# Kernel tuning notes

Measured on AMD Instinct MI355X. Metric: run time of the kernel, lower is better.

The kernel has to match this reference:

```python
import jax, jax.numpy as jnp
import numpy as np

N_NODES = 100000
N_EDGES = 1600000
N_GRAPHS = 256
D = 128
L = 3
N_OUT = 10


def setup_inputs() -> dict:
    key = jax.random.key(0)
    ks = jax.random.split(key, 6)
    x = jax.random.normal(ks[0], (N_NODES, D), dtype=jnp.float32)
    edge_index = jax.random.randint(ks[1], (2, N_EDGES), 0, N_NODES, dtype=jnp.int64)
    batch = jnp.sort(jax.random.randint(ks[2], (N_NODES,), 0, N_GRAPHS, dtype=jnp.int64))
    conv_w = jax.random.normal(ks[3], (L, D, D), dtype=jnp.float32) * (1.0 / np.sqrt(D))
    conv_b = jnp.zeros((L, D), dtype=jnp.float32)
    out_w = jax.random.normal(ks[4], (3 * D, N_OUT), dtype=jnp.float32) * (1.0 / np.sqrt(3 * D))
    out_b = jnp.zeros((N_OUT,), dtype=jnp.float32)
    return {"x": x, "edge_index": edge_index, "batch": batch,
            "conv_w": conv_w, "conv_b": conv_b, "out_w": out_w, "out_b": out_b}


def reference(x, edge_index, batch, conv_w, conv_b, out_w, out_b):
    N = x.shape[0]
    # --- add self-loops (PyG GCNConv default) ---
    loop = jnp.arange(N, dtype=edge_index.dtype)
    src = jnp.concatenate([edge_index[0], loop])  # [E+N]
    dst = jnp.concatenate([edge_index[1], loop])
    # --- symmetric normalization: deg computed on dst (col) ---
    deg = jax.ops.segment_sum(jnp.ones_like(dst, dtype=x.dtype), dst, num_segments=N)
    dinv = jnp.where(deg > 0, jax.lax.rsqrt(jnp.maximum(deg, 1.0)), 0.0)
    norm = dinv[src] * dinv[dst]  # [E+N]

    h = x
    for l in range(conv_w.shape[0]):
        h = h @ conv_w[l]                                   # [N, D] transform first
        msg = h[src] * norm[:, None]                        # gather + scale
        h = jax.ops.segment_sum(msg, dst, num_segments=N)   # scatter-add
        h = jax.nn.relu(h + conv_b[l])

    # --- global max / mean / add pooling over graphs ---
    B = N_GRAPHS
    gmax = jax.ops.segment_max(h, batch, num_segments=B)
    gsum = jax.ops.segment_sum(h, batch, num_segments=B)
    cnt = jax.ops.segment_sum(jnp.ones((N, 1), h.dtype), batch, num_segments=B)
    gmean = gsum / jnp.maximum(cnt, 1.0)
    pooled = jnp.concatenate([gmax, gmean, gsum], axis=1)   # [B, 3D]
    # dropout p=0.5 is identity in eval mode
    return pooled @ out_w + out_b
```

## Files before the change

kernel.cpp:

```cpp
#include <hip/hip_runtime.h>
#include <hip/hip_bf16.h>

#define D 128
#define NP 8
#define DPB 64
#define KPB (DPB * NP)
#define SUB 64
#define CAP_SUB 64

typedef __attribute__((ext_vector_type(8))) __bf16 bf16x8;
typedef __attribute__((ext_vector_type(4))) float f32x4;
typedef __attribute__((ext_vector_type(4))) short s16x4;
typedef __attribute__((ext_vector_type(8))) short s16x8;

static __device__ __forceinline__ short f2bf(float f) {
    union { float f; unsigned u; } in; in.f = f;
    unsigned u = in.u;
    u += 0x7fffu + ((u >> 16) & 1u);
    return (short)(u >> 16);
}

__global__ void k_bucket(const int* __restrict__ src, const int* __restrict__ dst,
                         int* __restrict__ bcnt, int* __restrict__ staging,
                         int E, int KBE) {
    int i = blockIdx.x * 256 + threadIdx.x;
    if (i >= E) return;
    int d = dst[i], s = src[i];
    int b = d >> 6;
    int key = ((d & 63) << 3) | (s >> 14);
    int j = blockIdx.x & (SUB - 1);
    int slot = atomicAdd(&bcnt[j * KBE + b], 1);
    if (slot < CAP_SUB) staging[((size_t)j * KBE + b) * CAP_SUB + slot] = (key << 17) | s;
}

__global__ void k_btot(const int* __restrict__ bcnt, int* __restrict__ btot, int KBE) {
    int b = blockIdx.x * 256 + threadIdx.x;
    if (b >= KBE) return;
    int v = 0;
    #pragma unroll
    for (int j = 0; j < SUB; j++) {
        int c = bcnt[j * KBE + b];
        v += (c > CAP_SUB) ? CAP_SUB : c;
    }
    btot[b] = v;
}

__global__ void k_bscan(const int* __restrict__ btot, int* __restrict__ bbase,
                        int* __restrict__ row_ptr, int nkeys, int KBE) {
    __shared__ int sm[512];
    __shared__ int carry;
    int t = threadIdx.x;
    if (t == 0) carry = 0;
    __syncthreads();
    for (int c0 = 0; c0 < KBE; c0 += 512) {
        int b = c0 + t;
        int v = (b < KBE) ? btot[b] : 0;
        sm[t] = v;
        __syncthreads();
        for (int off = 1; off < 512; off <<= 1) {
            int x = (t >= off) ? sm[t - off] : 0;
            __syncthreads();
            sm[t] += x;
            __syncthreads();
        }
        if (b < KBE) bbase[b] = sm[t] - v + carry;
        __syncthreads();
        if (t == 0) carry += sm[511];
        __syncthreads();
    }
    if (t == 0) { bbase[KBE] = carry; row_ptr[nkeys] = carry; }
}

__global__ __launch_bounds__(256) void k_build(
    const int* __restrict__ staging, const int* __restrict__ bcnt,
    const int* __restrict__ bbase, int* __restrict__ row_ptr,
    int* __restrict__ csr_src, float* __restrict__ dinv, int N, int KBE)
{
    const int b = blockIdx.x;
    const int tid = threadIdx.x;
    __shared__ int cnt[KPB];
    __shared__ int subn[SUB];
    __shared__ int chunkbuf[256];
    __shared__ int carry;

    if (tid < SUB) {
        int c = bcnt[tid * KBE + b];
        subn[tid] = (c > CAP_SUB) ? CAP_SUB : c;
    }
    for (int k = tid; k < KPB; k += 256) cnt[k] = 0;
    if (tid == 0) carry = 0;
    __syncthreads();

    const int base = bbase[b];
    const int nb = bbase[b + 1] - base;
    const int j = tid >> 2, l4 = tid & 3;
    const int* __restrict__ sreg = staging + ((size_t)j * KBE + b) * CAP_SUB;
    const int sn = subn[j];

    for (int e = l4; e < sn; e += 4)
        atomicAdd(&cnt[sreg[e] >> 17], 1);
    __syncthreads();

    #pragma unroll 1
    for (int c = 0; c < KPB / 256; c++) {
        int idx = c * 256 + tid;
        int v = cnt[idx];
        chunkbuf[tid] = v;
        __syncthreads();
        for (int off = 1; off < 256; off <<= 1) {
            int x = (tid >= off) ? chunkbuf[tid - off] : 0;
            __syncthreads();
            chunkbuf[tid] += x;
            __syncthreads();
        }
        cnt[idx] = chunkbuf[tid] - v + carry;
        __syncthreads();
        if (tid == 255) carry += chunkbuf[255];
        __syncthreads();
    }

    for (int k = tid; k < KPB; k += 256)
        row_ptr[(size_t)b * KPB + k] = base + cnt[k];
    for (int dl = tid; dl < DPB; dl += 256) {
        int d = b * DPB + dl;
        if (d < N) {
            int hi2 = (dl == DPB - 1) ? nb : cnt[(dl + 1) * NP];
            int deg = hi2 - cnt[dl * NP];
            dinv[d] = rsqrtf((float)deg + 1.0f);
        }
    }
    __syncthreads();

    for (int e = l4; e < sn; e += 4) {
        int w = sreg[e];
        int slot = base + atomicAdd(&cnt[w >> 17], 1);
        csr_src[slot] = w & 0x1FFFF;
    }
}

__global__ void k_gseg(const int* __restrict__ batch, int* __restrict__ gstart,
                       int* __restrict__ gcnt, int N, int B) {
    int g = blockIdx.x * blockDim.x + threadIdx.x;
    if (g > B) return;
    int lo = 0, hi = N;
    while (lo < hi) {
        int mid = (lo + hi) >> 1;
        if (batch[mid] < g) lo = mid + 1; else hi = mid;
    }
    gstart[g] = lo;
    if (g < B) {
        int lo2 = lo, hi2 = N;
        while (lo2 < hi2) {
            int mid = (lo2 + hi2) >> 1;
            if (batch[mid] < g + 1) lo2 = mid + 1; else hi2 = mid;
        }
        gcnt[g] = lo2 - lo;
    }
}

__global__ void k_cvt_x(const float* __restrict__ x, const float* __restrict__ dinv,
                        short* __restrict__ xb, int total4) {
    int i = blockIdx.x * blockDim.x + threadIdx.x;
    if (i < total4) {
        float d = dinv[i >> 5];
        float4 v = ((const float4*)x)[i];
        s16x4 o;
        o.x = f2bf(v.x * d); o.y = f2bf(v.y * d);
        o.z = f2bf(v.z * d); o.w = f2bf(v.w * d);
        ((s16x4*)xb)[i] = o;
    }
}

__global__ void k_cvt_w(const float* __restrict__ W, short* __restrict__ Wt, int total) {
    int i = blockIdx.x * blockDim.x + threadIdx.x;
    if (i < total) {
        int l = i >> 14;
        int rem = i & 16383;
        int n = rem >> 7;
        int k = rem & 127;
        Wt[i] = f2bf(W[(l << 14) + (k << 7) + n]);
    }
}

__global__ __launch_bounds__(256) void k_layer(
    const short* __restrict__ hin, const int* __restrict__ row_ptr,
    const int* __restrict__ csr_src, const float* __restrict__ dinv,
    const short* __restrict__ Wt, const float* __restrict__ bias,
    short* __restrict__ hout, float* __restrict__ hrelu, int N, int mode)
{
    __shared__ __align__(16) short tile[16 * 128];
    const int tid = threadIdx.x;
    const int wave = tid >> 6;
    const int lane = tid & 63;
    const int group = lane >> 4;
    const int lg = lane & 15;
    const int off = lg * 8;
    const int node_base = blockIdx.x * 16;
    const int r = wave * 4 + group;
    const int i = node_base + r;

    short* dstp = &tile[r * 128 + ((lg ^ (r & 7)) << 3)];
    if (i < N) {
        float acc[8];
        bf16x8 v = *(const bf16x8*)(hin + (size_t)i * D + off);
        #pragma unroll
        for (int k = 0; k < 8; k++) acc[k] = (float)v[k];

        int t = row_ptr[i * NP];
        const int end = row_ptr[i * NP + NP];
        const int nfull = (end - t) >> 3;

        int i0, i1, i2, i3, i4, i5, i6, i7;
        if (nfull > 0) {
            i0 = csr_src[t + 0]; i1 = csr_src[t + 1];
            i2 = csr_src[t + 2]; i3 = csr_src[t + 3];
            i4 = csr_src[t + 4]; i5 = csr_src[t + 5];
            i6 = csr_src[t + 6]; i7 = csr_src[t + 7];
        }
        #pragma unroll 1
        for (int c = 0; c < nfull; c++) {
            bf16x8 v0 = *(const bf16x8*)(hin + (size_t)i0 * D + off);
            bf16x8 v1 = *(const bf16x8*)(hin + (size_t)i1 * D + off);
            bf16x8 v2 = *(const bf16x8*)(hin + (size_t)i2 * D + off);
            bf16x8 v3 = *(const bf16x8*)(hin + (size_t)i3 * D + off);
            bf16x8 v4 = *(const bf16x8*)(hin + (size_t)i4 * D + off);
            bf16x8 v5 = *(const bf16x8*)(hin + (size_t)i5 * D + off);
            bf16x8 v6 = *(const bf16x8*)(hin + (size_t)i6 * D + off);
            bf16x8 v7 = *(const bf16x8*)(hin + (size_t)i7 * D + off);
            t += 8;
            if (c + 1 < nfull) {
                i0 = csr_src[t + 0]; i1 = csr_src[t + 1];
                i2 = csr_src[t + 2]; i3 = csr_src[t + 3];
                i4 = csr_src[t + 4]; i5 = csr_src[t + 5];
                i6 = csr_src[t + 6]; i7 = csr_src[t + 7];
            }
            #pragma unroll
            for (int k = 0; k < 8; k++)
                acc[k] += ((((float)v0[k] + (float)v1[k]) + ((float)v2[k] + (float)v3[k]))
                         + (((float)v4[k] + (float)v5[k]) + ((float)v6[k] + (float)v7[k])));
        }
        for (; t + 4 <= end; t += 4) {
            int j0 = csr_src[t + 0], j1 = csr_src[t + 1];
            int j2 = csr_src[t + 2], j3 = csr_src[t + 3];
            bf16x8 v0 = *(const bf16x8*)(hin + (size_t)j0 * D + off);
            bf16x8 v1 = *(const bf16x8*)(hin + (size_t)j1 * D + off);
            bf16x8 v2 = *(const bf16x8*)(hin + (size_t)j2 * D + off);
            bf16x8 v3 = *(const bf16x8*)(hin + (size_t)j3 * D + off);
            #pragma unroll
            for (int k = 0; k < 8; k++)
                acc[k] += (((float)v0[k] + (float)v1[k]) + ((float)v2[k] + (float)v3[k]));
        }
        for (; t < end; t++) {
            int j0 = csr_src[t];
            bf16x8 v0 = *(const bf16x8*)(hin + (size_t)j0 * D + off);
            #pragma unroll
            for (int k = 0; k < 8; k++) acc[k] += (float)v0[k];
        }

        const float di = dinv[i];
        s16x8 o;
        #pragma unroll
        for (int k = 0; k < 8; k++) o[k] = f2bf(acc[k] * di);
        *(s16x8*)dstp = o;
    } else {
        s16x8 z = {0, 0, 0, 0, 0, 0, 0, 0};
        *(s16x8*)dstp = z;
    }
    __syncthreads();

    bf16x8 afrag[4];
    #pragma unroll
    for (int kt = 0; kt < 4; kt++)
        afrag[kt] = *(const bf16x8*)(&tile[lg * 128 + (((group + 4 * kt) ^ (lg & 7)) << 3)]);

    f32x4 acc2[2];
    #pragma unroll
    for (int nt = 0; nt < 2; nt++) { f32x4 z = {0.f, 0.f, 0.f, 0.f}; acc2[nt] = z; }
    #pragma unroll
    for (int nt = 0; nt < 2; nt++) {
        const short* bp = Wt + (size_t)(wave * 32 + nt * 16 + lg) * D + group * 8;
        #pragma unroll
        for (int kt = 0; kt < 4; kt++) {
            bf16x8 b = *(const bf16x8*)(bp + kt * 32);
            acc2[nt] = __builtin_amdgcn_mfma_f32_16x16x32_bf16(afrag[kt], b, acc2[nt], 0, 0, 0);
        }
    }

    float bcol[2];
    #pragma unroll
    for (int nt = 0; nt < 2; nt++) bcol[nt] = bias[wave * 32 + nt * 16 + lg];
    const int row0 = node_base + group * 4;
    #pragma unroll
    for (int i2 = 0; i2 < 4; i2++) {
        int r2 = row0 + i2;
        if (r2 < N) {
            if (mode == 0) {
                float dr = dinv[r2];
                #pragma unroll
                for (int nt = 0; nt < 2; nt++) {
                    int col = wave * 32 + nt * 16 + lg;
                    float val = fmaxf(acc2[nt][i2] + bcol[nt], 0.0f);
                    hout[(size_t)r2 * D + col] = f2bf(val * dr);
                }
            } else {
                #pragma unroll
                for (int nt = 0; nt < 2; nt++) {
                    int col = wave * 32 + nt * 16 + lg;
                    hrelu[(size_t)r2 * D + col] = fmaxf(acc2[nt][i2] + bcol[nt], 0.0f);
                }
            }
        }
    }
}

__global__ __launch_bounds__(256) void k_pool(const float* __restrict__ hrelu,
                                              const int* __restrict__ gstart,
                                              const int* __restrict__ gcnt,
                                              float* __restrict__ pmax,
                                              float* __restrict__ psum, int B) {
    int g = blockIdx.x >> 2;
    int q = blockIdx.x & 3;
    int c = threadIdx.x & 127;
    int p = threadIdx.x >> 7;
    int start = gstart[g];
    int endr = start + gcnt[g];

    float mx0 = 0.f, mx1 = 0.f, sm0 = 0.f, sm1 = 0.f;
    int r = start + q * 2 + p;
    for (; r + 8 < endr; r += 16) {
        float v0 = hrelu[(size_t)r * D + c];
        float v1 = hrelu[(size_t)(r + 8) * D + c];
        mx0 = fmaxf(mx0, v0); sm0 += v0;
        mx1 = fmaxf(mx1, v1); sm1 += v1;
    }
    if (r < endr) {
        float v0 = hrelu[(size_t)r * D + c];
        mx0 = fmaxf(mx0, v0); sm0 += v0;
    }
    float mx = fmaxf(mx0, mx1), sm = sm0 + sm1;

    __shared__ float smx[128], ssm[128];
    if (p == 1) { smx[c] = mx; ssm[c] = sm; }
    __syncthreads();
    if (p == 0) {
        pmax[((size_t)q * B + g) * D + c] = fmaxf(mx, smx[c]);
        psum[((size_t)q * B + g) * D + c] = sm + ssm[c];
    }
}

__global__ void k_final(const float* __restrict__ pmax, const float* __restrict__ psum,
                        const int* __restrict__ gcnt, const float* __restrict__ ow,
                        const float* __restrict__ ob, float* __restrict__ out, int B) {
    int g = blockIdx.x;
    int t = threadIdx.x;
    float part[10];
    #pragma unroll
    for (int o = 0; o < 10; o++) part[o] = 0.f;
    float invc = 1.0f / fmaxf((float)gcnt[g], 1.0f);
    for (int k = t; k < 3 * D; k += 64) {
        int c = (k < D) ? k : ((k < 2 * D) ? k - D : k - 2 * D);
        float pk;
        if (k < D) {
            float m = pmax[(size_t)g * D + c];
            #pragma unroll
            for (int q = 1; q < 4; q++) m = fmaxf(m, pmax[((size_t)q * B + g) * D + c]);
            pk = m;
        } else {
            float s = psum[(size_t)g * D + c];
            #pragma unroll
            for (int q = 1; q < 4; q++) s += psum[((size_t)q * B + g) * D + c];
            pk = (k < 2 * D) ? s * invc : s;
        }
        const float* w = ow + k * 10;
        #pragma unroll
        for (int o = 0; o < 10; o++) part[o] += pk * w[o];
    }
    #pragma unroll
    for (int off = 32; off > 0; off >>= 1)
        #pragma unroll
        for (int o = 0; o < 10; o++) part[o] += __shfl_down(part[o], off, 64);
    if (t == 0)
        #pragma unroll
        for (int o = 0; o < 10; o++) out[g * 10 + o] = part[o] + ob[o];
}

extern "C" void kernel_launch(void* const* d_in, const int* in_sizes, int n_in,
                              void* d_out, int out_size, void* d_ws, size_t ws_size,
                              hipStream_t stream) {
    const float* x     = (const float*)d_in[0];
    const int*   ei    = (const int*)d_in[1];
    const int*   batch = (const int*)d_in[2];
    const float* convw = (const float*)d_in[3];
    const float* convb = (const float*)d_in[4];
    const float* outw  = (const float*)d_in[5];
    const float* outb  = (const float*)d_in[6];
    float* out = (float*)d_out;

    const int N = in_sizes[0] / D;
    const int E = in_sizes[1] / 2;
    const int L = in_sizes[3] / (D * D);
    const int B = out_size / 10;

    const int* src = ei;
    const int* dst = ei + E;

    const int KBE   = (N + DPB - 1) / DPB;
    const int nkeys = KBE * KPB;

    char* p = (char*)d_ws;
    auto alloc = [&](size_t bytes) { char* r = p; p += (bytes + 255) & ~255ull; return r; };
    short* hb0     = (short*)alloc((size_t)N * D * 2);
    short* hb1     = (short*)alloc((size_t)N * D * 2);
    float* hrelu   = (float*)alloc((size_t)N * D * 4);
    short* Wt      = (short*)alloc((size_t)L * D * D * 2);
    int*   row_ptr = (int*)alloc(((size_t)nkeys + 1) * 4);
    int*   csr_src = (int*)alloc((size_t)E * 4);
    int*   bcnt    = (int*)alloc((size_t)SUB * KBE * 4);
    int*   btot    = (int*)alloc((size_t)KBE * 4);
    int*   bbase   = (int*)alloc(((size_t)KBE + 1) * 4);
    float* dinv    = (float*)alloc((size_t)N * 4);
    float* pmax    = (float*)alloc((size_t)4 * B * D * 4);
    float* psum    = (float*)alloc((size_t)4 * B * D * 4);
    int*   gcnt    = (int*)alloc((size_t)B * 4);
    int*   gstart  = (int*)alloc(((size_t)B + 1) * 4);

    int* staging = (int*)hrelu;

    hipMemsetAsync(bcnt, 0, (size_t)SUB * KBE * 4, stream);

    k_bucket<<<(E + 255) / 256, 256, 0, stream>>>(src, dst, bcnt, staging, E, KBE);
    k_gseg<<<1, 512, 0, stream>>>(batch, gstart, gcnt, N, B);
    k_btot<<<(KBE + 255) / 256, 256, 0, stream>>>(bcnt, btot, KBE);
    k_bscan<<<1, 512, 0, stream>>>(btot, bbase, row_ptr, nkeys, KBE);
    k_build<<<KBE, 256, 0, stream>>>(staging, bcnt, bbase, row_ptr, csr_src, dinv, N, KBE);
    k_cvt_x<<<((N * D / 4) + 255) / 256, 256, 0, stream>>>(x, dinv, hb0, N * D / 4);
    k_cvt_w<<<((L * D * D) + 255) / 256, 256, 0, stream>>>(convw, Wt, L * D * D);

    const int lblocks = (N + 15) / 16;
    k_layer<<<lblocks, 256, 0, stream>>>(hb0, row_ptr, csr_src, dinv, Wt,
                                         convb, hb1, hrelu, N, 0);
    k_layer<<<lblocks, 256, 0, stream>>>(hb1, row_ptr, csr_src, dinv, Wt + D * D,
                                         convb + D, hb0, hrelu, N, 0);
    k_layer<<<lblocks, 256, 0, stream>>>(hb0, row_ptr, csr_src, dinv, Wt + 2 * D * D,
                                         convb + 2 * D, hb1, hrelu, N, 1);

    k_pool<<<B * 4, 256, 0, stream>>>(hrelu, gstart, gcnt, pmax, psum, B);
    k_final<<<B, 64, 0, stream>>>(pmax, psum, gcnt, outw, outb, out, B);
}
```

Before: 458.1 us.

## Replace bucketed source-sorted CSR build with plain histogram-scan-scatter CSR

```diff
diff --git a/kernel.cpp b/kernel.cpp
--- a/kernel.cpp
+++ b/kernel.cpp
@@ -2,11 +2,6 @@
 #include <hip/hip_bf16.h>
 
 #define D 128
-#define NP 8
-#define DPB 64
-#define KPB (DPB * NP)
-#define SUB 64
-#define CAP_SUB 64
 
 typedef __attribute__((ext_vector_type(8))) __bf16 bf16x8;
 typedef __attribute__((ext_vector_type(4))) float f32x4;
@@ -20,122 +15,64 @@
     return (short)(u >> 16);
 }
 
-__global__ void k_bucket(const int* __restrict__ src, const int* __restrict__ dst,
-                         int* __restrict__ bcnt, int* __restrict__ staging,
-                         int E, int KBE) {
+
+__global__ void k_hist(const int* __restrict__ dst, int* __restrict__ cnt, int E) {
+    int i = blockIdx.x * 256 + threadIdx.x;
+    if (i < E) atomicAdd(&cnt[dst[i]], 1);
+}
+
+__global__ void k_scan1(const int* __restrict__ cnt, int* __restrict__ row_ptr,
+                        int* __restrict__ part, int N) {
+    __shared__ int sm[256];
+    const int t = threadIdx.x;
+    const int i = blockIdx.x * 256 + t;
+    int v = (i < N) ? cnt[i] : 0;
+    sm[t] = v;
+    __syncthreads();
+    for (int off = 1; off < 256; off <<= 1) {
+        int x = (t >= off) ? sm[t - off] : 0;
+        __syncthreads();
+        sm[t] += x;
+        __syncthreads();
+    }
+    if (i < N) row_ptr[i] = sm[t] - v;
+    if (t == 255) part[blockIdx.x] = sm[255];
+}
+
+__global__ void k_scan2(int* __restrict__ part, int nb) {
+    __shared__ int sm[512];
+    const int t = threadIdx.x;
+    int v = (t < nb) ? part[t] : 0;
+    sm[t] = v;
+    __syncthreads();
+    for (int off = 1; off < 512; off <<= 1) {
+        int x = (t >= off) ? sm[t - off] : 0;
+        __syncthreads();
+        sm[t] += x;
+        __syncthreads();
+    }
+    if (t < nb) part[t] = sm[t] - v;
+}
+
+__global__ void k_scan3(const int* __restrict__ cnt, int* __restrict__ row_ptr,
+                        const int* __restrict__ part, int* __restrict__ cur,
+                        float* __restrict__ dinv, int N, int E) {
+    const int i = blockIdx.x * 256 + threadIdx.x;
+    if (i < N) {
+        int r = row_ptr[i] + part[blockIdx.x];
+        row_ptr[i] = r;
+        cur[i] = r;
+        dinv[i] = rsqrtf((float)cnt[i] + 1.0f);
+    }
+    if (blockIdx.x == 0 && threadIdx.x == 0) row_ptr[N] = E;
+}
+
+__global__ void k_scatter(const int* __restrict__ src, const int* __restrict__ dst,
+                          int* __restrict__ cur, int* __restrict__ csr_src, int E) {
     int i = blockIdx.x * 256 + threadIdx.x;
     if (i >= E) return;
-    int d = dst[i], s = src[i];
-    int b = d >> 6;
-    int key = ((d & 63) << 3) | (s >> 14);
-    int j = blockIdx.x & (SUB - 1);
-    int slot = atomicAdd(&bcnt[j * KBE + b], 1);
-    if (slot < CAP_SUB) staging[((size_t)j * KBE + b) * CAP_SUB + slot] = (key << 17) | s;
-}
-
-__global__ void k_btot(const int* __restrict__ bcnt, int* __restrict__ btot, int KBE) {
-    int b = blockIdx.x * 256 + threadIdx.x;
-    if (b >= KBE) return;
-    int v = 0;
-    #pragma unroll
-    for (int j = 0; j < SUB; j++) {
-        int c = bcnt[j * KBE + b];
-        v += (c > CAP_SUB) ? CAP_SUB : c;
-    }
-    btot[b] = v;
-}
-
-__global__ void k_bscan(const int* __restrict__ btot, int* __restrict__ bbase,
-                        int* __restrict__ row_ptr, int nkeys, int KBE) {
-    __shared__ int sm[512];
-    __shared__ int carry;
-    int t = threadIdx.x;
-    if (t == 0) carry = 0;
-    __syncthreads();
-    for (int c0 = 0; c0 < KBE; c0 += 512) {
-        int b = c0 + t;
-        int v = (b < KBE) ? btot[b] : 0;
-        sm[t] = v;
-        __syncthreads();
-        for (int off = 1; off < 512; off <<= 1) {
-            int x = (t >= off) ? sm[t - off] : 0;
-            __syncthreads();
-            sm[t] += x;
-            __syncthreads();
-        }
-        if (b < KBE) bbase[b] = sm[t] - v + carry;
-        __syncthreads();
-        if (t == 0) carry += sm[511];
-        __syncthreads();
-    }
-    if (t == 0) { bbase[KBE] = carry; row_ptr[nkeys] = carry; }
-}
-
-__global__ __launch_bounds__(256) void k_build(
-    const int* __restrict__ staging, const int* __restrict__ bcnt,
-    const int* __restrict__ bbase, int* __restrict__ row_ptr,
-    int* __restrict__ csr_src, float* __restrict__ dinv, int N, int KBE)
-{
-    const int b = blockIdx.x;
-    const int tid = threadIdx.x;
-    __shared__ int cnt[KPB];
-    __shared__ int subn[SUB];
-    __shared__ int chunkbuf[256];
-    __shared__ int carry;
-
-    if (tid < SUB) {
-        int c = bcnt[tid * KBE + b];
-        subn[tid] = (c > CAP_SUB) ? CAP_SUB : c;
-    }
-    for (int k = tid; k < KPB; k += 256) cnt[k] = 0;
-    if (tid == 0) carry = 0;
-    __syncthreads();
-
-    const int base = bbase[b];
-    const int nb = bbase[b + 1] - base;
-    const int j = tid >> 2, l4 = tid & 3;
-    const int* __restrict__ sreg = staging + ((size_t)j * KBE + b) * CAP_SUB;
-    const int sn = subn[j];
-
-    for (int e = l4; e < sn; e += 4)
-        atomicAdd(&cnt[sreg[e] >> 17], 1);
-    __syncthreads();
-
-    #pragma unroll 1
-    for (int c = 0; c < KPB / 256; c++) {
-        int idx = c * 256 + tid;
-        int v = cnt[idx];
-        chunkbuf[tid] = v;
-        __syncthreads();
-        for (int off = 1; off < 256; off <<= 1) {
-            int x = (tid >= off) ? chunkbuf[tid - off] : 0;
-            __syncthreads();
-            chunkbuf[tid] += x;
-            __syncthreads();
-        }
-        cnt[idx] = chunkbuf[tid] - v + carry;
-        __syncthreads();
-        if (tid == 255) carry += chunkbuf[255];
-        __syncthreads();
-    }
-
-    for (int k = tid; k < KPB; k += 256)
-        row_ptr[(size_t)b * KPB + k] = base + cnt[k];
-    for (int dl = tid; dl < DPB; dl += 256) {
-        int d = b * DPB + dl;
-        if (d < N) {
-            int hi2 = (dl == DPB - 1) ? nb : cnt[(dl + 1) * NP];
-            int deg = hi2 - cnt[dl * NP];
-            dinv[d] = rsqrtf((float)deg + 1.0f);
-        }
-    }
-    __syncthreads();
-
-    for (int e = l4; e < sn; e += 4) {
-        int w = sreg[e];
-        int slot = base + atomicAdd(&cnt[w >> 17], 1);
-        csr_src[slot] = w & 0x1FFFF;
-    }
+    int pos = atomicAdd(&cur[dst[i]], 1);
+    csr_src[pos] = src[i];
 }
 
 __global__ void k_gseg(const int* __restrict__ batch, int* __restrict__ gstart,
@@ -206,8 +143,8 @@
         #pragma unroll
         for (int k = 0; k < 8; k++) acc[k] = (float)v[k];
 
-        int t = row_ptr[i * NP];
-        const int end = row_ptr[i * NP + NP];
+        int t = row_ptr[i];
+        const int end = row_ptr[i + 1];
         const int nfull = (end - t) >> 3;
 
         int i0, i1, i2, i3, i4, i5, i6, i7;
@@ -404,35 +341,33 @@
     const int* src = ei;
     const int* dst = ei + E;
 
-    const int KBE   = (N + DPB - 1) / DPB;
-    const int nkeys = KBE * KPB;
-
     char* p = (char*)d_ws;
     auto alloc = [&](size_t bytes) { char* r = p; p += (bytes + 255) & ~255ull; return r; };
     short* hb0     = (short*)alloc((size_t)N * D * 2);
     short* hb1     = (short*)alloc((size_t)N * D * 2);
     float* hrelu   = (float*)alloc((size_t)N * D * 4);
     short* Wt      = (short*)alloc((size_t)L * D * D * 2);
-    int*   row_ptr = (int*)alloc(((size_t)nkeys + 1) * 4);
+    int*   row_ptr = (int*)alloc(((size_t)N + 1) * 4);
     int*   csr_src = (int*)alloc((size_t)E * 4);
-    int*   bcnt    = (int*)alloc((size_t)SUB * KBE * 4);
-    int*   btot    = (int*)alloc((size_t)KBE * 4);
-    int*   bbase   = (int*)alloc(((size_t)KBE + 1) * 4);
+    int*   cnt     = (int*)alloc((size_t)N * 4);
+    int*   cur     = (int*)alloc((size_t)N * 4);
+    int*   part    = (int*)alloc(1024 * 4);
     float* dinv    = (float*)alloc((size_t)N * 4);
     float* pmax    = (float*)alloc((size_t)4 * B * D * 4);
     float* psum    = (float*)alloc((size_t)4 * B * D * 4);
     int*   gcnt    = (int*)alloc((size_t)B * 4);
     int*   gstart  = (int*)alloc(((size_t)B + 1) * 4);
 
-    int* staging = (int*)hrelu;
-
-    hipMemsetAsync(bcnt, 0, (size_t)SUB * KBE * 4, stream);
-
-    k_bucket<<<(E + 255) / 256, 256, 0, stream>>>(src, dst, bcnt, staging, E, KBE);
+    const int nb = (N + 255) / 256;
+
+    hipMemsetAsync(cnt, 0, (size_t)N * 4, stream);
+
+    k_hist<<<(E + 255) / 256, 256, 0, stream>>>(dst, cnt, E);
     k_gseg<<<1, 512, 0, stream>>>(batch, gstart, gcnt, N, B);
-    k_btot<<<(KBE + 255) / 256, 256, 0, stream>>>(bcnt, btot, KBE);
-    k_bscan<<<1, 512, 0, stream>>>(btot, bbase, row_ptr, nkeys, KBE);
-    k_build<<<KBE, 256, 0, stream>>>(staging, bcnt, bbase, row_ptr, csr_src, dinv, N, KBE);
+    k_scan1<<<nb, 256, 0, stream>>>(cnt, row_ptr, part, N);
+    k_scan2<<<1, 512, 0, stream>>>(part, nb);
+    k_scan3<<<nb, 256, 0, stream>>>(cnt, row_ptr, part, cur, dinv, N, E);
+    k_scatter<<<(E + 255) / 256, 256, 0, stream>>>(src, dst, cur, csr_src, E);
     k_cvt_x<<<((N * D / 4) + 255) / 256, 256, 0, stream>>>(x, dinv, hb0, N * D / 4);
     k_cvt_w<<<((L * D * D) + 255) / 256, 256, 0, stream>>>(convw, Wt, L * D * D);
 
```

New measurement: 564.1 us. 23.1% more time.
